# Kernel optimization log

Measured on AMD Instinct MI355X. Metric: run time of the kernel, lower is better.

## Reference

```python
import jax, jax.numpy as jnp
import numpy as np
from jax import lax

B, H, W, C, NH = 16, 56, 56, 192, 6
L = H * W
DH = C // NH            # 32
HID = 4 * C             # 768
ETA = 1.0 / DH          # TTT inner-loop learning rate
EPS = 1e-5

# ---- RoPE rotation tables (deterministic buffer, shape (H, W, C//2)) ----
_kmax = C // 4
_theta = 1.0 / (10000.0 ** (np.arange(_kmax) / _kmax))
_ii, _jj = np.meshgrid(np.arange(H), np.arange(W), indexing='ij')
_ang = np.concatenate([_ii[..., None] * _theta, _jj[..., None] * _theta], axis=-1)  # (H,W,C/2)
_COS = jnp.asarray(np.cos(_ang), dtype=jnp.float32)
_SIN = jnp.asarray(np.sin(_ang), dtype=jnp.float32)


def layernorm(x, g, b):
    mu = jnp.mean(x, axis=-1, keepdims=True)
    var = jnp.mean(jnp.square(x - mu), axis=-1, keepdims=True)
    return (x - mu) * lax.rsqrt(var + EPS) * g + b


def dwconv3x3(x_blc, w, b):
    # x: (B, L, Ch) -> depthwise 3x3 conv over (H, W) -> (B, L, Ch)
    Ch = x_blc.shape[-1]
    xi = x_blc.reshape(B, H, W, Ch).transpose(0, 3, 1, 2)  # NCHW
    y = lax.conv_general_dilated(xi, w, (1, 1), 'SAME', feature_group_count=Ch,
                                 dimension_numbers=('NCHW', 'OIHW', 'NCHW'))
    y = y + b[None, :, None, None]
    return y.transpose(0, 2, 3, 1).reshape(B, L, Ch)


def rope(x):
    # x: (B, L, C); rotate complex pairs with 2D axial angles
    xr = x.reshape(B, H, W, C // 2, 2)
    re, im = xr[..., 0], xr[..., 1]
    o_re = _COS * re - _SIN * im
    o_im = _SIN * re + _COS * im
    return jnp.stack([o_re, o_im], axis=-1).reshape(B, L, C)


def ttt_attn(xn, qkv_w, qkv_b, W0, proj_w, proj_b):
    qkv = xn @ qkv_w.T + qkv_b                      # (B, L, 3C)
    q, k, v = jnp.split(qkv, 3, axis=-1)
    q = rope(q) * (DH ** -0.5)
    k = rope(k)

    def to_heads(t):  # (B,L,C) -> (L, B*NH, DH)
        return t.reshape(B, L, NH, DH).transpose(1, 0, 2, 3).reshape(L, B * NH, DH)
    qs, ks, vs = to_heads(q), to_heads(k), to_heads(v)

    Wst0 = jnp.broadcast_to(W0[None], (B, NH, DH, DH)).reshape(B * NH, DH, DH)

    def step(Wst, qkv_t):
        qt, kt, vt = qkv_t
        pred = jnp.einsum('bij,bj->bi', Wst, kt)
        Wn = Wst - ETA * (pred - vt)[:, :, None] * kt[:, None, :]
        ot = jnp.einsum('bij,bj->bi', Wn, qt)
        return Wn, ot

    _, out = lax.scan(step, Wst0, (qs, ks, vs))     # out: (L, B*NH, DH)
    out = out.reshape(L, B, NH, DH).transpose(1, 0, 2, 3).reshape(B, L, C)
    return out @ proj_w.T + proj_b


def setup_inputs() -> dict:
    key = jax.random.key(0)
    ks = jax.random.split(key, 12)
    s = 0.02
    return {
        'x': jax.random.normal(ks[0], (B, L, C), jnp.float32),
        'cpe_w': jax.random.normal(ks[1], (C, 1, 3, 3), jnp.float32) * s,
        'cpe_b': jnp.zeros((C,), jnp.float32),
        'n1_g': jnp.ones((C,), jnp.float32),
        'n1_b': jnp.zeros((C,), jnp.float32),
        'qkv_w': jax.random.normal(ks[2], (3 * C, C), jnp.float32) * s,
        'qkv_b': jnp.zeros((3 * C,), jnp.float32),
        'W0': jax.random.normal(ks[3], (NH, DH, DH), jnp.float32) * s,
        'proj_w': jax.random.normal(ks[4], (C, C), jnp.float32) * s,
        'proj_b': jnp.zeros((C,), jnp.float32),
        'n2_g': jnp.ones((C,), jnp.float32),
        'n2_b': jnp.zeros((C,), jnp.float32),
        'fc1_w': jax.random.normal(ks[5], (HID, C), jnp.float32) * s,
        'fc1_b': jnp.zeros((HID,), jnp.float32),
        'dwc_w': jax.random.normal(ks[6], (HID, 1, 3, 3), jnp.float32) * s,
        'dwc_b': jnp.zeros((HID,), jnp.float32),
        'fc2_w': jax.random.normal(ks[7], (C, HID), jnp.float32) * s,
        'fc2_b': jnp.zeros((C,), jnp.float32),
    }


def reference(x, cpe_w, cpe_b, n1_g, n1_b, qkv_w, qkv_b, W0, proj_w, proj_b,
              n2_g, n2_b, fc1_w, fc1_b, dwc_w, dwc_b, fc2_w, fc2_b):
    # CPE: conditional positional encoding (depthwise conv residual)
    x = x + dwconv3x3(x, cpe_w, cpe_b)
    # TTT attention branch
    x = x + ttt_attn(layernorm(x, n1_g, n1_b), qkv_w, qkv_b, W0, proj_w, proj_b)
    # MLP branch with depthwise conv
    h1 = jax.nn.gelu(layernorm(x, n2_g, n2_b) @ fc1_w.T + fc1_b, approximate=False)
    h1 = jax.nn.gelu(h1 + dwconv3x3(h1, dwc_w, dwc_b), approximate=False)
    x = x + (h1 @ fc2_w.T + fc2_b)
    return x
```

## Files before the change

kernel.cpp:

```cpp
#include <hip/hip_runtime.h>
#include <hip/hip_bf16.h>

#define Bc 16
#define Hc 56
#define Wcc 56
#define Cc 192
#define NHc 6
#define Lc 3136
#define DHc 32
#define HIDc 768
#define NHEAD 96
#define Sc 32
#define NCHUNK 98
#define NPAIR (NHEAD*NCHUNK)
#define ROWS (Bc*Lc)
#define GR2 (ROWS/2)
#define ETAc (1.0f/32.0f)

typedef unsigned short u16;
typedef unsigned int u32;
typedef __attribute__((ext_vector_type(8))) short bf16x8;
typedef __attribute__((ext_vector_type(4))) float f32x4;
typedef __attribute__((ext_vector_type(16))) float f32x16;

__device__ __forceinline__ float b2f(u16 v){ u32 u = ((u32)v)<<16; float f; __builtin_memcpy(&f,&u,4); return f; }
__device__ __forceinline__ u16 f2b(float f){ u32 u; __builtin_memcpy(&u,&f,4); u32 r = u + 0x7FFFu + ((u>>16)&1u); return (u16)(r>>16); }
__device__ __forceinline__ f32x16 zero16(){ f32x16 z = {0,0,0,0,0,0,0,0,0,0,0,0,0,0,0,0}; return z; }

__device__ __forceinline__ void make_bfrags(const f32x16& t, int hi, bf16x8& b1, bf16x8& b2){
  u32 P[8], S[8];
  #pragma unroll
  for (int q=0;q<4;q++){
    #pragma unroll
    for (int j=0;j<2;j++){
      u32 r; float lo = t[4*q+2*j], hv = t[4*q+2*j+1];
      asm("v_cvt_pk_bf16_f32 %0, %1, %2" : "=v"(r) : "v"(lo), "v"(hv));
      P[2*q+j] = r;
    }
  }
  #pragma unroll
  for (int i=0;i<8;i++) S[i] = (u32)__shfl_xor((int)P[i], 32);
  union { u32 u[4]; bf16x8 v; } f1, f2;
  if (hi==0){ f1.u[0]=P[0]; f1.u[1]=P[1]; f1.u[2]=S[0]; f1.u[3]=S[1];
              f2.u[0]=P[4]; f2.u[1]=P[5]; f2.u[2]=S[4]; f2.u[3]=S[5]; }
  else      { f1.u[0]=S[2]; f1.u[1]=S[3]; f1.u[2]=P[2]; f1.u[3]=P[3];
              f2.u[0]=S[6]; f2.u[1]=S[7]; f2.u[2]=P[6]; f2.u[3]=P[7]; }
  b1 = f1.v; b2 = f2.v;
}

__global__ __launch_bounds__(256) void prep_kernel(
    const float* __restrict__ qkvw, const float* __restrict__ projw,
    const float* __restrict__ fc1w, const float* __restrict__ fc2w,
    const float* __restrict__ dwcw, const float* __restrict__ cpew,
    u16* __restrict__ wbqkv, u16* __restrict__ wbproj, u16* __restrict__ wbfc1,
    u16* __restrict__ wbfc2, float* __restrict__ dwt9, float* __restrict__ cwt9){
  int i = blockIdx.x*256 + threadIdx.x;
  if (i < 110592) wbqkv[i] = f2b(qkvw[i]);
  else if (i < 147456){ int j=i-110592; wbproj[j] = f2b(projw[j]); }
  else if (i < 294912){ int j=i-147456; wbfc1[j] = f2b(fc1w[j]); }
  else if (i < 442368){ int j=i-294912; wbfc2[j] = f2b(fc2w[j]); }
  else if (i < 449280){ int j=i-442368; int ch=j/9, t=j-ch*9; dwt9[t*HIDc+ch] = dwcw[j]; }
  else if (i < 451008){ int j=i-449280; int ch=j/9, t=j-ch*9; cwt9[t*Cc+ch] = cpew[j]; }
}

__global__ __launch_bounds__(256) void rope_tab_kernel(float* __restrict__ ct, float* __restrict__ st){
  int i = blockIdx.x*256 + threadIdx.x;
  int l = i/96, p = i - l*96;
  int h = l/Wcc, w = l - h*Wcc;
  int kk = (p<48)? p : p-48;
  float th = powf(10000.f, -(float)kk/48.f);
  float ang = (float)((p<48)? h : w) * th;
  ct[i] = cosf(ang);
  st[i] = sinf(ang);
}

__global__ __launch_bounds__(192) void cpe_ln_kernel(const float* __restrict__ x, const float* __restrict__ cwt9,
                                                     const float* __restrict__ bs, const float* __restrict__ g,
                                                     const float* __restrict__ b,
                                                     u16* __restrict__ x1, u16* __restrict__ xn){
  __shared__ float ps[192], pq[192], smu[8], srs[8];
  int tid = threadIdx.x;
  int rl = tid/24, sub = tid - rl*24, ch0 = sub*8;
  int row = blockIdx.x*8 + rl;
  int l = row % Lc; int h = l/Wcc, w = l - h*Wcc;
  const float* xp = x + (size_t)row*Cc + ch0;
  float acc[8];
  { f32x4 b0 = *(const f32x4*)(bs+ch0), b1v = *(const f32x4*)(bs+ch0+4);
    acc[0]=b0[0];acc[1]=b0[1];acc[2]=b0[2];acc[3]=b0[3];
    acc[4]=b1v[0];acc[5]=b1v[1];acc[6]=b1v[2];acc[7]=b1v[3]; }
  #pragma unroll
  for (int kh=0;kh<3;kh++){
    int hh = h+kh-1; if (hh<0 || hh>=Hc) continue;
    #pragma unroll
    for (int kw=0;kw<3;kw++){
      int ww = w+kw-1; if (ww<0 || ww>=Wcc) continue;
      const float* ip = xp + ((kh-1)*Wcc + (kw-1))*Cc;
      f32x4 i0 = *(const f32x4*)ip, i1 = *(const f32x4*)(ip+4);
      const float* wp = cwt9 + (kh*3+kw)*Cc + ch0;
      f32x4 w0 = *(const f32x4*)wp, w1 = *(const f32x4*)(wp+4);
      acc[0] += i0[0]*w0[0]; acc[1] += i0[1]*w0[1]; acc[2] += i0[2]*w0[2]; acc[3] += i0[3]*w0[3];
      acc[4] += i1[0]*w1[0]; acc[5] += i1[1]*w1[1]; acc[6] += i1[2]*w1[2]; acc[7] += i1[3]*w1[3];
    }
  }
  float val[8];
  { f32x4 c0 = *(const f32x4*)xp, c1 = *(const f32x4*)(xp+4);
    val[0]=c0[0]+acc[0]; val[1]=c0[1]+acc[1]; val[2]=c0[2]+acc[2]; val[3]=c0[3]+acc[3];
    val[4]=c1[0]+acc[4]; val[5]=c1[1]+acc[5]; val[6]=c1[2]+acc[6]; val[7]=c1[3]+acc[7]; }
  float s8=0.f, q8=0.f;
  #pragma unroll
  for (int j=0;j<8;j++){ s8 += val[j]; q8 += val[j]*val[j]; }
  ps[tid]=s8; pq[tid]=q8;
  __syncthreads();
  if (tid < 8){
    float s=0.f, q=0.f;
    #pragma unroll
    for (int k=0;k<24;k++){ s += ps[tid*24+k]; q += pq[tid*24+k]; }
    float mu = s*(1.f/Cc);
    float var = q*(1.f/Cc) - mu*mu;
    smu[tid] = mu; srs[tid] = rsqrtf(var + 1e-5f);
  }
  __syncthreads();
  float mu = smu[rl], rstd = srs[rl];
  union { bf16x8 v; u16 s[8]; } o1, o2;
  f32x4 g0 = *(const f32x4*)(g+ch0), g1 = *(const f32x4*)(g+ch0+4);
  f32x4 bb0 = *(const f32x4*)(b+ch0), bb1 = *(const f32x4*)(b+ch0+4);
  float gg[8] = {g0[0],g0[1],g0[2],g0[3],g1[0],g1[1],g1[2],g1[3]};
  float bbv[8] = {bb0[0],bb0[1],bb0[2],bb0[3],bb1[0],bb1[1],bb1[2],bb1[3]};
  #pragma unroll
  for (int j=0;j<8;j++){
    o1.s[j] = f2b(val[j]);
    o2.s[j] = f2b((val[j]-mu)*rstd*gg[j] + bbv[j]);
  }
  *(bf16x8*)(x1 + (size_t)row*Cc + ch0) = o1.v;
  *(bf16x8*)(xn + (size_t)row*Cc + ch0) = o2.v;
}

__global__ __launch_bounds__(256) void ln_kernel(const u16* __restrict__ xb, const float* __restrict__ g,
                                                 const float* __restrict__ b, u16* __restrict__ out){
  int row = blockIdx.x*4 + (threadIdx.x>>6);
  int lane = threadIdx.x & 63;
  const u16* xr = xb + (size_t)row*Cc;
  float v0 = b2f(xr[lane]), v1 = b2f(xr[lane+64]), v2 = b2f(xr[lane+128]);
  float s = v0+v1+v2;
  float q = v0*v0 + v1*v1 + v2*v2;
  #pragma unroll
  for (int off=32; off; off>>=1){ s += __shfl_xor(s, off); q += __shfl_xor(q, off); }
  float mu = s*(1.f/Cc);
  float var = q*(1.f/Cc) - mu*mu;
  float rstd = rsqrtf(var + 1e-5f);
  u16* orow = out + (size_t)row*Cc;
  orow[lane]     = f2b((v0-mu)*rstd*g[lane]     + b[lane]);
  orow[lane+64]  = f2b((v1-mu)*rstd*g[lane+64]  + b[lane+64]);
  orow[lane+128] = f2b((v2-mu)*rstd*g[lane+128] + b[lane+128]);
}

template<int MODE, int KT>
__global__ __launch_bounds__(256) void gemm_kernel(
    const u16* __restrict__ A, const u16* __restrict__ Wt,
    const float* __restrict__ bias,
    float* __restrict__ outf, u16* __restrict__ outb, u16* __restrict__ vdst,
    const u16* __restrict__ residb,
    const float* __restrict__ ct, const float* __restrict__ st,
    u16* __restrict__ q_s, u16* __restrict__ k_s)
{
  constexpr int NCH = KT/192;
  __shared__ __align__(16) char smem[64*200*2];
  u16* As = (u16*)smem;
  float* Os32 = (float*)smem;
  u16* Osu = (u16*)smem;
  int tid = threadIdx.x;
  int wid = tid>>6, lane = tid&63;
  int wr = wid>>1, wc = wid&1;
  int m0 = blockIdx.x*64;
  int nblk = blockIdx.y*192;
  int n0 = nblk + wc*96;
  int ar = lane&15, kg = lane>>4;
  f32x4 acc[2][6];
  #pragma unroll
  for (int f=0;f<2;f++)
    #pragma unroll
    for (int c=0;c<6;c++){ f32x4 z = {0.f,0.f,0.f,0.f}; acc[f][c] = z; }
  bf16x8 bcur[6], bnxt[6];
  #pragma unroll
  for (int c=0;c<6;c++) bcur[c] = *(const bf16x8*)(Wt + (size_t)(n0 + c*16 + ar)*KT + kg*8);
  #pragma unroll
  for (int ch=0; ch<NCH; ch++){
    if (ch>0) __syncthreads();
    #pragma unroll
    for (int j=0;j<6;j++){
      int g = j*256 + tid;
      int grow = g/24, gcol = (g - grow*24)*8;
      bf16x8 v = *(const bf16x8*)(A + (size_t)(m0+grow)*KT + ch*192 + gcol);
      *(bf16x8*)(As + grow*200 + gcol) = v;
    }
    __syncthreads();
    #pragma unroll
    for (int kc=0;kc<6;kc++){
      int s = ch*6 + kc;
      if (s+1 < NCH*6){
        int koff = ((s+1)/6)*192 + ((s+1)%6)*32 + kg*8;
        #pragma unroll
        for (int c=0;c<6;c++) bnxt[c] = *(const bf16x8*)(Wt + (size_t)(n0 + c*16 + ar)*KT + koff);
      }
      bf16x8 af[2];
      #pragma unroll
      for (int f=0;f<2;f++)
        af[f] = *(const bf16x8*)(As + (wr*32 + f*16 + ar)*200 + kc*32 + kg*8);
      #pragma unroll
      for (int f=0;f<2;f++)
        #pragma unroll
        for (int c=0;c<6;c++)
          acc[f][c] = __builtin_amdgcn_mfma_f32_16x16x32_bf16(af[f], bcur[c], acc[f][c], 0,0,0);
      #pragma unroll
      for (int c=0;c<6;c++) bcur[c] = bnxt[c];
    }
  }
  __syncthreads();
  if (MODE != 3){
    #pragma unroll
    for (int f=0;f<2;f++){
      #pragma unroll
      for (int c=0;c<6;c++){
        float bv = bias[n0 + c*16 + ar];
        #pragma unroll
        for (int j=0;j<4;j++){
          float v = acc[f][c][j] + bv;
          if (MODE==2) v = 0.5f*v*(1.f + erff(v*0.70710678118654752f));
          Osu[(wr*32 + f*16 + kg*4 + j)*200 + wc*96 + c*16 + ar] = f2b(v);
        }
      }
    }
    __syncthreads();
    #pragma unroll
    for (int j=0;j<6;j++){
      int g = j*256 + tid;
      int grow = g/24, gcol = (g - grow*24)*8;
      bf16x8 v = *(const bf16x8*)(Osu + grow*200 + gcol);
      int row = m0 + grow;
      if (MODE==2){
        *(bf16x8*)(outb + (size_t)row*HIDc + nblk + gcol) = v;
      } else if (MODE==1){
        const u16* rp = residb + (size_t)row*Cc + gcol;
        bf16x8 rv = *(const bf16x8*)rp;
        union { bf16x8 v; u16 s[8]; } o;
        #pragma unroll
        for (int t=0;t<8;t++) o.s[t] = f2b(b2f((u16)v[t]) + b2f((u16)rv[t]));
        *(bf16x8*)(outb + (size_t)row*Cc + gcol) = o.v;
      } else {
        int bb = row/Lc; int l = row - bb*Lc;
        int nh = gcol>>5, d = gcol&31;
        if (nblk < 384){
          bool isq = (nblk == 0);
          int p0 = gcol>>1;
          f32x4 cv = *(const f32x4*)(ct + l*96 + p0);
          f32x4 sv = *(const f32x4*)(st + l*96 + p0);
          float sc = isq ? 0.1767766952966369f : 1.0f;
          union { bf16x8 v; u16 s[8]; } o;
          #pragma unroll
          for (int t=0;t<4;t++){
            float re = b2f((u16)v[2*t]), im = b2f((u16)v[2*t+1]);
            o.s[2*t]   = f2b((cv[t]*re - sv[t]*im)*sc);
            o.s[2*t+1] = f2b((sv[t]*re + cv[t]*im)*sc);
          }
          u16* dst = (isq ? q_s : k_s) + (((size_t)(bb*NHc+nh))*Lc + l)*DHc + d;
          *(bf16x8*)dst = o.v;
        } else {
          *(bf16x8*)(vdst + (((size_t)(bb*NHc+nh))*Lc + l)*DHc + d) = v;
        }
      }
    }
  } else {
    #pragma unroll
    for (int half=0; half<2; half++){
      if (wc==half){
        #pragma unroll
        for (int f=0;f<2;f++){
          #pragma unroll
          for (int c=0;c<6;c++){
            float bv = bias[n0 + c*16 + ar];
            #pragma unroll
            for (int j=0;j<4;j++)
              Os32[(wr*32 + f*16 + kg*4 + j)*100 + c*16 + ar] = acc[f][c][j] + bv;
          }
        }
      }
      __syncthreads();
      #pragma unroll
      for (int j=0;j<6;j++){
        int g = j*256 + tid;
        int grow = g/24, qcol = (g - grow*24)*4;
        f32x4 v = *(const f32x4*)(Os32 + grow*100 + qcol);
        int row = m0 + grow, colg = half*96 + qcol;
        const u16* rp = residb + (size_t)row*Cc + colg;
        v[0] += b2f(rp[0]); v[1] += b2f(rp[1]); v[2] += b2f(rp[2]); v[3] += b2f(rp[3]);
        *(f32x4*)(outf + (size_t)row*Cc + colg) = v;
      }
      if (half==0) __syncthreads();
    }
  }
}

__global__ __launch_bounds__(64) void ttta_kernel(const u16* __restrict__ k_s, const u16* __restrict__ v_s,
                                                  u16* __restrict__ u_s, u16* __restrict__ rn_s,
                                                  u16* __restrict__ af_s, u16* __restrict__ bc_s){
  __shared__ float Gl[1024];
  __shared__ u16 LK[32*40];
  __shared__ float LU[32*33];
  __shared__ float LR[32*33];
  int pair = blockIdx.x;
  int head = pair / NCHUNK;
  int l0 = (pair - head*NCHUNK) * Sc;
  int lane = threadIdx.x; int rr = lane&31; int hi = lane>>5; int ks = hi*8;
  const u16* kb = k_s + ((size_t)head*Lc + l0)*DHc;
  bf16x8 a0 = *(const bf16x8*)(kb + rr*32 + ks);
  bf16x8 a1 = *(const bf16x8*)(kb + rr*32 + 16 + ks);
  *(bf16x8*)(LK + rr*40 + ks) = a0;
  *(bf16x8*)(LK + rr*40 + 16 + ks) = a1;
  f32x16 g = zero16();
  g = __builtin_amdgcn_mfma_f32_32x32x16_bf16(a0, a0, g, 0,0,0);
  g = __builtin_amdgcn_mfma_f32_32x32x16_bf16(a1, a1, g, 0,0,0);
  #pragma unroll
  for (int reg=0;reg<16;reg++){
    int i = (reg&3) + 8*(reg>>2) + 4*hi;
    Gl[i*32 + rr] = ETAc * g[reg];
  }
  __syncthreads();
  float X[32];
  if (lane < 32){
    #pragma unroll
    for (int i=0;i<32;i++) X[i] = ETAc * b2f(v_s[((size_t)head*Lc + l0 + i)*DHc + lane]);
  } else {
    int m = lane-32;
    #pragma unroll
    for (int i=0;i<32;i++) X[i] = ETAc * b2f(kb[i*32 + m]);
  }
  #pragma unroll
  for (int i=1;i<32;i++){
    float a = X[i];
    #pragma unroll
    for (int j=0;j<i;j++) a -= Gl[i*32+j]*X[j];
    X[i] = a;
  }
  if (lane < 32){
    u16* dst = u_s + (size_t)pair*1024 + lane;
    #pragma unroll
    for (int i=0;i<32;i++) dst[i*32] = f2b(X[i]);
    #pragma unroll
    for (int i=0;i<32;i++) LU[lane*33 + i] = X[i];
  } else {
    u16* dst = rn_s + (size_t)pair*1024 + (lane&31);
    #pragma unroll
    for (int i=0;i<32;i++) dst[i*32] = f2b(-X[i]);
    #pragma unroll
    for (int i=0;i<32;i++) LR[(lane&31)*33 + i] = X[i];
  }
  __syncthreads();
  union { bf16x8 v; u16 s[8]; } kc1, kc2, uc1, uc2, rc1, rc2;
  #pragma unroll
  for (int s=0;s<8;s++){
    kc1.s[s] = LK[(ks+s)*40 + rr];
    kc2.s[s] = LK[(16+ks+s)*40 + rr];
    uc1.s[s] = f2b(LU[rr*33 + ks+s]);
    uc2.s[s] = f2b(LU[rr*33 + 16+ks+s]);
    rc1.s[s] = f2b(LR[rr*33 + ks+s]);
    rc2.s[s] = f2b(LR[rr*33 + 16+ks+s]);
  }
  f32x16 bacc = zero16();
  bacc = __builtin_amdgcn_mfma_f32_32x32x16_bf16(kc1.v, uc1.v, bacc, 0,0,0);
  bacc = __builtin_amdgcn_mfma_f32_32x32x16_bf16(kc2.v, uc2.v, bacc, 0,0,0);
  union { bf16x8 v; u16 s[8]; } bo1, bo2;
  #pragma unroll
  for (int r=0;r<8;r++){ bo1.s[r] = f2b(bacc[r]); bo2.s[r] = f2b(bacc[8+r]); }
  *(bf16x8*)(bc_s + (size_t)pair*1024 + lane*16) = bo1.v;
  *(bf16x8*)(bc_s + (size_t)pair*1024 + lane*16 + 8) = bo2.v;
  f32x16 aacc = zero16();
  aacc = __builtin_amdgcn_mfma_f32_32x32x16_bf16(rc1.v, kc1.v, aacc, 0,0,0);
  aacc = __builtin_amdgcn_mfma_f32_32x32x16_bf16(rc2.v, kc2.v, aacc, 0,0,0);
  f32x16 an;
  #pragma unroll
  for (int r=0;r<16;r++) an[r] = -aacc[r];
  bf16x8 f1, f2;
  make_bfrags(an, hi, f1, f2);
  *(bf16x8*)(af_s + (size_t)pair*1024 + lane*16) = f1;
  *(bf16x8*)(af_s + (size_t)pair*1024 + lane*16 + 8) = f2;
}

__global__ __launch_bounds__(64) void tttb_kernel(const u16* __restrict__ af_s, const u16* __restrict__ bc_s,
                                                  const float* __restrict__ W0, u16* __restrict__ w_snap){
  int head = blockIdx.x; int nh = head % NHc;
  int lane = threadIdx.x; int rr = lane&31; int hi = lane>>5;
  f32x16 T;
  const float* w0r = W0 + nh*1024 + rr*32 + 4*hi;
  #pragma unroll
  for (int q=0;q<4;q++){
    f32x4 v = *(const f32x4*)(w0r + 8*q);
    T[4*q+0]=v[0]; T[4*q+1]=v[1]; T[4*q+2]=v[2]; T[4*q+3]=v[3];
  }
  size_t hb = (size_t)head*NCHUNK;
  const bf16x8* afp = (const bf16x8*)(af_s + hb*1024);
  const bf16x8* bcp = (const bf16x8*)(bc_s + hb*1024);
  bf16x8 A1 = afp[lane*2], A2 = afp[lane*2+1];
  bf16x8 Bv1 = bcp[lane*2], Bv2 = bcp[lane*2+1];
  bf16x8 b1, b2;
  make_bfrags(T, hi, b1, b2);
  for (int c=0;c<NCHUNK;c++){
    bf16x8 nA1=A1, nA2=A2, nB1=Bv1, nB2=Bv2;
    if (c+1 < NCHUNK){
      int base = (c+1)*128 + lane*2;
      nA1 = afp[base]; nA2 = afp[base+1];
      nB1 = bcp[base]; nB2 = bcp[base+1];
    }
    u16* wrow = w_snap + (hb + c)*1024 + rr*32;
    *(bf16x8*)(wrow + hi*8) = b1;
    *(bf16x8*)(wrow + 16 + hi*8) = b2;
    f32x16 acc;
    #pragma unroll
    for (int r=0;r<8;r++){ acc[r] = T[r] + b2f((u16)Bv1[r]); acc[8+r] = T[8+r] + b2f((u16)Bv2[r]); }
    acc = __builtin_amdgcn_mfma_f32_32x32x16_bf16(A1, b1, acc, 0,0,0);
    acc = __builtin_amdgcn_mfma_f32_32x32x16_bf16(A2, b2, acc, 0,0,0);
    T = acc;
    make_bfrags(T, hi, b1, b2);
    A1=nA1; A2=nA2; Bv1=nB1; Bv2=nB2;
  }
}

__global__ __launch_bounds__(64) void tttc_kernel(const u16* __restrict__ q_s, const u16* __restrict__ k_s,
                                                  const u16* __restrict__ w_snap, const u16* __restrict__ u_s,
                                                  const u16* __restrict__ rn_s, u16* __restrict__ o_bf){
  __shared__ __align__(16) u16 Pl[32*40];
  int pair = blockIdx.x;
  int head = pair / NCHUNK;
  int ch = pair - head*NCHUNK;
  int l0 = ch*Sc;
  int lane = threadIdx.x; int rr = lane&31; int hi = lane>>5; int ks = hi*8;
  const u16* qb = q_s + ((size_t)head*Lc + l0)*DHc;
  const u16* kb = k_s + ((size_t)head*Lc + l0)*DHc;
  bf16x8 q0 = *(const bf16x8*)(qb + rr*32 + ks);
  bf16x8 q1 = *(const bf16x8*)(qb + rr*32 + 16 + ks);
  bf16x8 k0 = *(const bf16x8*)(kb + rr*32 + ks);
  bf16x8 k1 = *(const bf16x8*)(kb + rr*32 + 16 + ks);
  f32x16 p = zero16();
  p = __builtin_amdgcn_mfma_f32_32x32x16_bf16(q0, k0, p, 0,0,0);
  p = __builtin_amdgcn_mfma_f32_32x32x16_bf16(q1, k1, p, 0,0,0);
  #pragma unroll
  for (int reg=0;reg<16;reg++){
    int i = (reg&3)+8*(reg>>2)+4*hi;
    Pl[i*40+rr] = (rr<=i) ? f2b(p[reg]) : (u16)0;
  }
  const u16* wsb = w_snap + (size_t)pair*1024;
  bf16x8 tb0 = *(const bf16x8*)(wsb + rr*32 + ks);
  bf16x8 tb1 = *(const bf16x8*)(wsb + rr*32 + 16 + ks);
  const u16* ub = u_s + (size_t)pair*1024;
  f32x16 wr;
  #pragma unroll
  for (int r=0;r<16;r++){
    int i = (r&3)+8*(r>>2)+4*hi;
    wr[r] = b2f(ub[i*32 + rr]);
  }
  const u16* rb = rn_s + (size_t)pair*1024;
  bf16x8 rn0 = *(const bf16x8*)(rb + rr*32 + ks);
  bf16x8 rn1 = *(const bf16x8*)(rb + rr*32 + 16 + ks);
  wr = __builtin_amdgcn_mfma_f32_32x32x16_bf16(rn0, tb0, wr, 0,0,0);
  wr = __builtin_amdgcn_mfma_f32_32x32x16_bf16(rn1, tb1, wr, 0,0,0);
  bf16x8 wb0, wb1;
  make_bfrags(wr, hi, wb0, wb1);
  __syncthreads();
  f32x16 o = zero16();
  o = __builtin_amdgcn_mfma_f32_32x32x16_bf16(q0, tb0, o, 0,0,0);
  o = __builtin_amdgcn_mfma_f32_32x32x16_bf16(q1, tb1, o, 0,0,0);
  bf16x8 pa0 = *(const bf16x8*)(Pl + rr*40 + ks);
  bf16x8 pa1 = *(const bf16x8*)(Pl + rr*40 + 16 + ks);
  o = __builtin_amdgcn_mfma_f32_32x32x16_bf16(pa0, wb0, o, 0,0,0);
  o = __builtin_amdgcn_mfma_f32_32x32x16_bf16(pa1, wb1, o, 0,0,0);
  int bb = head/NHc, nh = head - bb*NHc;
  #pragma unroll
  for (int reg=0;reg<16;reg++){
    int i = (reg&3)+8*(reg>>2)+4*hi;
    o_bf[((size_t)(bb*Lc + l0 + i))*Cc + nh*32 + rr] = f2b(o[reg]);
  }
}

__global__ __launch_bounds__(256) void dwc_kernel(const u16* __restrict__ h1, const float* __restrict__ wt9,
                                                  const float* __restrict__ bs, u16* __restrict__ h2, int row0){
  int gid = blockIdx.x*256 + threadIdx.x;
  int cg = gid % 96; int lrow = gid / 96; int ch0 = cg*8;
  int row = row0 + lrow;
  int l = row % Lc; int h = l/Wcc, w = l - h*Wcc;
  const u16* hp = h1 + (size_t)lrow*HIDc + ch0;
  float acc[8];
  { f32x4 b0 = *(const f32x4*)(bs+ch0), b1v = *(const f32x4*)(bs+ch0+4);
    acc[0]=b0[0];acc[1]=b0[1];acc[2]=b0[2];acc[3]=b0[3];
    acc[4]=b1v[0];acc[5]=b1v[1];acc[6]=b1v[2];acc[7]=b1v[3]; }
  #pragma unroll
  for (int kh=0;kh<3;kh++){
    int hh = h+kh-1; if (hh<0 || hh>=Hc) continue;
    #pragma unroll
    for (int kw=0;kw<3;kw++){
      int ww = w+kw-1; if (ww<0 || ww>=Wcc) continue;
      bf16x8 iv = *(const bf16x8*)(hp + ((kh-1)*Wcc + (kw-1))*HIDc);
      const float* wp = wt9 + (kh*3+kw)*HIDc + ch0;
      f32x4 w0 = *(const f32x4*)wp, w1 = *(const f32x4*)(wp+4);
      acc[0] += b2f((u16)iv[0])*w0[0]; acc[1] += b2f((u16)iv[1])*w0[1];
      acc[2] += b2f((u16)iv[2])*w0[2]; acc[3] += b2f((u16)iv[3])*w0[3];
      acc[4] += b2f((u16)iv[4])*w1[0]; acc[5] += b2f((u16)iv[5])*w1[1];
      acc[6] += b2f((u16)iv[6])*w1[2]; acc[7] += b2f((u16)iv[7])*w1[3];
    }
  }
  bf16x8 cv = *(const bf16x8*)hp;
  union { bf16x8 v; u16 s[8]; } ov;
  #pragma unroll
  for (int j=0;j<8;j++){
    float v = b2f((u16)cv[j]) + acc[j];
    ov.s[j] = f2b(0.5f*v*(1.f + erff(v*0.70710678118654752f)));
  }
  *(bf16x8*)(h2 + (size_t)lrow*HIDc + ch0) = ov.v;
}

extern "C" void kernel_launch(void* const* d_in, const int* in_sizes, int n_in,
                              void* d_out, int out_size, void* d_ws, size_t ws_size,
                              hipStream_t stream){
  const float* x     = (const float*)d_in[0];
  const float* cpe_w = (const float*)d_in[1];
  const float* cpe_b = (const float*)d_in[2];
  const float* n1_g  = (const float*)d_in[3];
  const float* n1_b  = (const float*)d_in[4];
  const float* qkv_w = (const float*)d_in[5];
  const float* qkv_b = (const float*)d_in[6];
  const float* W0    = (const float*)d_in[7];
  const float* proj_w= (const float*)d_in[8];
  const float* proj_b= (const float*)d_in[9];
  const float* n2_g  = (const float*)d_in[10];
  const float* n2_b  = (const float*)d_in[11];
  const float* fc1_w = (const float*)d_in[12];
  const float* fc1_b = (const float*)d_in[13];
  const float* dwc_w = (const float*)d_in[14];
  const float* dwc_b = (const float*)d_in[15];
  const float* fc2_w = (const float*)d_in[16];
  const float* fc2_b = (const float*)d_in[17];

  char* ws = (char*)d_ws;
  size_t off = 0;
  auto alloc = [&](size_t bytes)->char*{
    char* p = ws + off;
    off += (bytes + 255) & ~(size_t)255;
    return p;
  };
  u16* wbqkv = (u16*)alloc((size_t)576*192*2);
  u16* wbproj= (u16*)alloc((size_t)192*192*2);
  u16* wbfc1 = (u16*)alloc((size_t)768*192*2);
  u16* wbfc2 = (u16*)alloc((size_t)192*768*2);
  float* dwt9 = (float*)alloc((size_t)9*HIDc*4);
  float* cwt9 = (float*)alloc((size_t)9*Cc*4);
  float* ctab = (float*)alloc((size_t)Lc*96*4);
  float* stab = (float*)alloc((size_t)Lc*96*4);
  u16* regA = (u16*)alloc((size_t)ROWS*Cc*2);
  u16* regB = (u16*)alloc((size_t)ROWS*Cc*2);
  u16* regC = (u16*)alloc((size_t)NHEAD*Lc*DHc*2);
  u16* regD = (u16*)alloc((size_t)NHEAD*Lc*DHc*2);
  u16* regE = (u16*)alloc((size_t)NHEAD*Lc*DHc*2);
  u16* rn_s = (u16*)alloc((size_t)NPAIR*1024*2);
  u16* af_s = (u16*)alloc((size_t)NPAIR*1024*2);
  u16* us = (u16*)d_out;
  u16* bc = us + (size_t)NPAIR*1024;

  u16* x1 = regA;
  u16* x2b = regA;
  u16* xn = regB;
  u16* obf = regB;
  u16* xn2 = regB;
  u16* qs = regC;
  u16* vs = regD;
  u16* wsn = regD;
  u16* ksb = regE;
  u16* h1 = regD;
  u16* h2 = rn_s;

  prep_kernel<<<(451008+255)/256,256,0,stream>>>(qkv_w, proj_w, fc1_w, fc2_w, dwc_w, cpe_w,
                                                 wbqkv, wbproj, wbfc1, wbfc2, dwt9, cwt9);
  rope_tab_kernel<<<(Lc*96)/256,256,0,stream>>>(ctab, stab);

  cpe_ln_kernel<<<ROWS/8,192,0,stream>>>(x, cwt9, cpe_b, n1_g, n1_b, x1, xn);
  { dim3 g(ROWS/64, 3); gemm_kernel<0,192><<<g,256,0,stream>>>(xn, wbqkv, qkv_b,
      nullptr, nullptr, vs, nullptr, ctab, stab, qs, ksb); }
  ttta_kernel<<<NPAIR,64,0,stream>>>(ksb, vs, us, rn_s, af_s, bc);
  tttb_kernel<<<NHEAD,64,0,stream>>>(af_s, bc, W0, wsn);
  tttc_kernel<<<NPAIR,64,0,stream>>>(qs, ksb, wsn, us, rn_s, obf);
  { dim3 g(ROWS/64, 1); gemm_kernel<1,192><<<g,256,0,stream>>>(obf, wbproj, proj_b,
      nullptr, x2b, nullptr, x1, nullptr, nullptr, nullptr, nullptr); }
  ln_kernel<<<ROWS/4,256,0,stream>>>(x2b, n2_g, n2_b, xn2);
  for (int g4=0; g4<2; g4++){
    const u16* a_in = xn2 + (size_t)g4*GR2*Cc;
    float* xo = (float*)d_out + (size_t)g4*GR2*Cc;
    const u16* res = x2b + (size_t)g4*GR2*Cc;
    { dim3 g(GR2/64, 4); gemm_kernel<2,192><<<g,256,0,stream>>>(a_in, wbfc1, fc1_b,
        nullptr, h1, nullptr, nullptr, nullptr, nullptr, nullptr, nullptr); }
    dwc_kernel<<<(GR2*96)/256,256,0,stream>>>(h1, dwt9, dwc_b, h2, g4*GR2);
    { dim3 g(GR2/64, 1); gemm_kernel<3,768><<<g,256,0,stream>>>(h2, wbfc2, fc2_b,
        xo, nullptr, nullptr, res, nullptr, nullptr, nullptr, nullptr); }
  }
}
```

Baseline: 503.3 us.

## Fuse depthwise conv into fc2 GEMM and loop N-blocks inside GEMM blocks

The standalone depthwise-conv+GELU kernel is folded into the fc2 GEMM: each 32-row block computes the conv output for all 768 channels directly into shared memory and then runs the K=768 MFMA loop from there. This removes the h2 round trip through global memory and one launch per half. The generic GEMM now loads its A tile once and loops over all N-blocks (3 for qkv, 4 for fc1) inside one block, so A is not reloaded per grid column. The cost is fewer, longer blocks, a larger shared-memory footprint that may lower occupancy, and 32-row fc2 tiles with less MFMA reuse.

```diff
diff --git a/kernel.cpp b/kernel.cpp
--- a/kernel.cpp
+++ b/kernel.cpp
@@ -154,53 +154,46 @@
   orow[lane+128] = f2b((v2-mu)*rstd*g[lane+128] + b[lane+128]);
 }
 
-template<int MODE, int KT>
+template<int MODE, int NB>
 __global__ __launch_bounds__(256) void gemm_kernel(
     const u16* __restrict__ A, const u16* __restrict__ Wt,
     const float* __restrict__ bias,
-    float* __restrict__ outf, u16* __restrict__ outb, u16* __restrict__ vdst,
+    u16* __restrict__ outb, u16* __restrict__ vdst,
     const u16* __restrict__ residb,
     const float* __restrict__ ct, const float* __restrict__ st,
     u16* __restrict__ q_s, u16* __restrict__ k_s)
 {
-  constexpr int NCH = KT/192;
-  __shared__ __align__(16) char smem[64*200*2];
-  u16* As = (u16*)smem;
-  float* Os32 = (float*)smem;
-  u16* Osu = (u16*)smem;
+  __shared__ __align__(16) u16 As[64*200];
+  __shared__ __align__(16) u16 Osu[64*200];
   int tid = threadIdx.x;
   int wid = tid>>6, lane = tid&63;
   int wr = wid>>1, wc = wid&1;
   int m0 = blockIdx.x*64;
-  int nblk = blockIdx.y*192;
-  int n0 = nblk + wc*96;
   int ar = lane&15, kg = lane>>4;
-  f32x4 acc[2][6];
-  #pragma unroll
-  for (int f=0;f<2;f++)
-    #pragma unroll
-    for (int c=0;c<6;c++){ f32x4 z = {0.f,0.f,0.f,0.f}; acc[f][c] = z; }
-  bf16x8 bcur[6], bnxt[6];
-  #pragma unroll
-  for (int c=0;c<6;c++) bcur[c] = *(const bf16x8*)(Wt + (size_t)(n0 + c*16 + ar)*KT + kg*8);
-  #pragma unroll
-  for (int ch=0; ch<NCH; ch++){
-    if (ch>0) __syncthreads();
-    #pragma unroll
-    for (int j=0;j<6;j++){
-      int g = j*256 + tid;
-      int grow = g/24, gcol = (g - grow*24)*8;
-      bf16x8 v = *(const bf16x8*)(A + (size_t)(m0+grow)*KT + ch*192 + gcol);
-      *(bf16x8*)(As + grow*200 + gcol) = v;
-    }
-    __syncthreads();
+  #pragma unroll
+  for (int j=0;j<6;j++){
+    int g = j*256 + tid;
+    int grow = g/24, gcol = (g - grow*24)*8;
+    *(bf16x8*)(As + grow*200 + gcol) = *(const bf16x8*)(A + (size_t)(m0+grow)*192 + gcol);
+  }
+  __syncthreads();
+  #pragma unroll
+  for (int nb=0; nb<NB; nb++){
+    const int nblk = nb*192;
+    const int n0 = nblk + wc*96;
+    f32x4 acc[2][6];
+    #pragma unroll
+    for (int f=0;f<2;f++)
+      #pragma unroll
+      for (int c=0;c<6;c++){ f32x4 z={0.f,0.f,0.f,0.f}; acc[f][c]=z; }
+    bf16x8 bcur[6], bnxt[6];
+    #pragma unroll
+    for (int c=0;c<6;c++) bcur[c] = *(const bf16x8*)(Wt + (size_t)(n0 + c*16 + ar)*192 + kg*8);
     #pragma unroll
     for (int kc=0;kc<6;kc++){
-      int s = ch*6 + kc;
-      if (s+1 < NCH*6){
-        int koff = ((s+1)/6)*192 + ((s+1)%6)*32 + kg*8;
+      if (kc < 5){
         #pragma unroll
-        for (int c=0;c<6;c++) bnxt[c] = *(const bf16x8*)(Wt + (size_t)(n0 + c*16 + ar)*KT + koff);
+        for (int c=0;c<6;c++) bnxt[c] = *(const bf16x8*)(Wt + (size_t)(n0 + c*16 + ar)*192 + (kc+1)*32 + kg*8);
       }
       bf16x8 af[2];
       #pragma unroll
@@ -214,9 +207,7 @@
       #pragma unroll
       for (int c=0;c<6;c++) bcur[c] = bnxt[c];
     }
-  }
-  __syncthreads();
-  if (MODE != 3){
+    __syncthreads();
     #pragma unroll
     for (int f=0;f<2;f++){
       #pragma unroll
@@ -240,8 +231,7 @@
       if (MODE==2){
         *(bf16x8*)(outb + (size_t)row*HIDc + nblk + gcol) = v;
       } else if (MODE==1){
-        const u16* rp = residb + (size_t)row*Cc + gcol;
-        bf16x8 rv = *(const bf16x8*)rp;
+        bf16x8 rv = *(const bf16x8*)(residb + (size_t)row*Cc + gcol);
         union { bf16x8 v; u16 s[8]; } o;
         #pragma unroll
         for (int t=0;t<8;t++) o.s[t] = f2b(b2f((u16)v[t]) + b2f((u16)rv[t]));
@@ -249,8 +239,8 @@
       } else {
         int bb = row/Lc; int l = row - bb*Lc;
         int nh = gcol>>5, d = gcol&31;
-        if (nblk < 384){
-          bool isq = (nblk == 0);
+        if (nb < 2){
+          const bool isq = (nb == 0);
           int p0 = gcol>>1;
           f32x4 cv = *(const f32x4*)(ct + l*96 + p0);
           f32x4 sv = *(const f32x4*)(st + l*96 + p0);
@@ -269,33 +259,99 @@
         }
       }
     }
-  } else {
-    #pragma unroll
-    for (int half=0; half<2; half++){
-      if (wc==half){
+  }
+}
+
+__global__ __launch_bounds__(256) void dwcfc2_kernel(
+    const u16* __restrict__ h1, const float* __restrict__ wt9, const float* __restrict__ dbs,
+    const u16* __restrict__ Wt, const float* __restrict__ bias,
+    const u16* __restrict__ residb, float* __restrict__ outf)
+{
+  __shared__ __align__(16) u16 As[32*776];
+  __shared__ __align__(16) float Os32[32*100];
+  int tid = threadIdx.x;
+  int wid = tid>>6, lane = tid&63;
+  int wr = wid>>1, wc = wid&1;
+  int m0 = blockIdx.x*32;
+  int n0 = wc*96;
+  int ar = lane&15, kg = lane>>4;
+  #pragma unroll
+  for (int j=0;j<12;j++){
+    int g = j*256 + tid;
+    int grow = g/96, gcol = (g - grow*96)*8;
+    int row = m0 + grow;
+    int l = row % Lc; int h = l/Wcc, w = l - h*Wcc;
+    const u16* hp = h1 + (size_t)row*HIDc + gcol;
+    float acc[8];
+    { f32x4 b0 = *(const f32x4*)(dbs+gcol), b1v = *(const f32x4*)(dbs+gcol+4);
+      acc[0]=b0[0];acc[1]=b0[1];acc[2]=b0[2];acc[3]=b0[3];
+      acc[4]=b1v[0];acc[5]=b1v[1];acc[6]=b1v[2];acc[7]=b1v[3]; }
+    #pragma unroll
+    for (int kh=0;kh<3;kh++){
+      int hh = h+kh-1; if (hh<0 || hh>=Hc) continue;
+      #pragma unroll
+      for (int kw=0;kw<3;kw++){
+        int ww = w+kw-1; if (ww<0 || ww>=Wcc) continue;
+        bf16x8 iv = *(const bf16x8*)(hp + ((kh-1)*Wcc + (kw-1))*HIDc);
+        const float* wp = wt9 + (kh*3+kw)*HIDc + gcol;
+        f32x4 w0 = *(const f32x4*)wp, w1 = *(const f32x4*)(wp+4);
+        acc[0] += b2f((u16)iv[0])*w0[0]; acc[1] += b2f((u16)iv[1])*w0[1];
+        acc[2] += b2f((u16)iv[2])*w0[2]; acc[3] += b2f((u16)iv[3])*w0[3];
+        acc[4] += b2f((u16)iv[4])*w1[0]; acc[5] += b2f((u16)iv[5])*w1[1];
+        acc[6] += b2f((u16)iv[6])*w1[2]; acc[7] += b2f((u16)iv[7])*w1[3];
+      }
+    }
+    bf16x8 cv = *(const bf16x8*)hp;
+    union { bf16x8 v; u16 s[8]; } ov;
+    #pragma unroll
+    for (int t=0;t<8;t++){
+      float v = b2f((u16)cv[t]) + acc[t];
+      ov.s[t] = f2b(0.5f*v*(1.f + erff(v*0.70710678118654752f)));
+    }
+    *(bf16x8*)(As + grow*776 + gcol) = ov.v;
+  }
+  __syncthreads();
+  f32x4 acc[6];
+  #pragma unroll
+  for (int c=0;c<6;c++){ f32x4 z={0.f,0.f,0.f,0.f}; acc[c]=z; }
+  bf16x8 bcur[6], bnxt[6];
+  #pragma unroll
+  for (int c=0;c<6;c++) bcur[c] = *(const bf16x8*)(Wt + (size_t)(n0 + c*16 + ar)*HIDc + kg*8);
+  #pragma unroll
+  for (int ks=0; ks<24; ks++){
+    if (ks < 23){
+      #pragma unroll
+      for (int c=0;c<6;c++) bnxt[c] = *(const bf16x8*)(Wt + (size_t)(n0 + c*16 + ar)*HIDc + (ks+1)*32 + kg*8);
+    }
+    bf16x8 af = *(const bf16x8*)(As + (wr*16 + ar)*776 + ks*32 + kg*8);
+    #pragma unroll
+    for (int c=0;c<6;c++)
+      acc[c] = __builtin_amdgcn_mfma_f32_16x16x32_bf16(af, bcur[c], acc[c], 0,0,0);
+    #pragma unroll
+    for (int c=0;c<6;c++) bcur[c] = bnxt[c];
+  }
+  #pragma unroll
+  for (int half=0; half<2; half++){
+    __syncthreads();
+    if (wc==half){
+      #pragma unroll
+      for (int c=0;c<6;c++){
+        float bv = bias[n0 + c*16 + ar];
         #pragma unroll
-        for (int f=0;f<2;f++){
-          #pragma unroll
-          for (int c=0;c<6;c++){
-            float bv = bias[n0 + c*16 + ar];
-            #pragma unroll
-            for (int j=0;j<4;j++)
-              Os32[(wr*32 + f*16 + kg*4 + j)*100 + c*16 + ar] = acc[f][c][j] + bv;
-          }
-        }
+        for (int j=0;j<4;j++)
+          Os32[(wr*16 + kg*4 + j)*100 + c*16 + ar] = acc[c][j] + bv;
       }
-      __syncthreads();
-      #pragma unroll
-      for (int j=0;j<6;j++){
-        int g = j*256 + tid;
-        int grow = g/24, qcol = (g - grow*24)*4;
-        f32x4 v = *(const f32x4*)(Os32 + grow*100 + qcol);
-        int row = m0 + grow, colg = half*96 + qcol;
-        const u16* rp = residb + (size_t)row*Cc + colg;
-        v[0] += b2f(rp[0]); v[1] += b2f(rp[1]); v[2] += b2f(rp[2]); v[3] += b2f(rp[3]);
-        *(f32x4*)(outf + (size_t)row*Cc + colg) = v;
-      }
-      if (half==0) __syncthreads();
+    }
+    __syncthreads();
+    #pragma unroll
+    for (int j=0;j<3;j++){
+      int g = j*256 + tid;
+      int grow = g/24, qcol = (g - grow*24)*4;
+      f32x4 v = *(const f32x4*)(Os32 + grow*100 + qcol);
+      int row = m0 + grow, colg = half*96 + qcol;
+      const u16* rp = residb + (size_t)row*Cc + colg;
+      v[0] += b2f(rp[0]); v[1] += b2f(rp[1]); v[2] += b2f(rp[2]); v[3] += b2f(rp[3]);
+      *(f32x4*)(outf + (size_t)row*Cc + colg) = v;
     }
   }
 }
@@ -478,42 +534,6 @@
     int i = (reg&3)+8*(reg>>2)+4*hi;
     o_bf[((size_t)(bb*Lc + l0 + i))*Cc + nh*32 + rr] = f2b(o[reg]);
   }
-}
-
-__global__ __launch_bounds__(256) void dwc_kernel(const u16* __restrict__ h1, const float* __restrict__ wt9,
-                                                  const float* __restrict__ bs, u16* __restrict__ h2, int row0){
-  int gid = blockIdx.x*256 + threadIdx.x;
-  int cg = gid % 96; int lrow = gid / 96; int ch0 = cg*8;
-  int row = row0 + lrow;
-  int l = row % Lc; int h = l/Wcc, w = l - h*Wcc;
-  const u16* hp = h1 + (size_t)lrow*HIDc + ch0;
-  float acc[8];
-  { f32x4 b0 = *(const f32x4*)(bs+ch0), b1v = *(const f32x4*)(bs+ch0+4);
-    acc[0]=b0[0];acc[1]=b0[1];acc[2]=b0[2];acc[3]=b0[3];
-    acc[4]=b1v[0];acc[5]=b1v[1];acc[6]=b1v[2];acc[7]=b1v[3]; }
-  #pragma unroll
-  for (int kh=0;kh<3;kh++){
-    int hh = h+kh-1; if (hh<0 || hh>=Hc) continue;
-    #pragma unroll
-    for (int kw=0;kw<3;kw++){
-      int ww = w+kw-1; if (ww<0 || ww>=Wcc) continue;
-      bf16x8 iv = *(const bf16x8*)(hp + ((kh-1)*Wcc + (kw-1))*HIDc);
-      const float* wp = wt9 + (kh*3+kw)*HIDc + ch0;
-      f32x4 w0 = *(const f32x4*)wp, w1 = *(const f32x4*)(wp+4);
-      acc[0] += b2f((u16)iv[0])*w0[0]; acc[1] += b2f((u16)iv[1])*w0[1];
-      acc[2] += b2f((u16)iv[2])*w0[2]; acc[3] += b2f((u16)iv[3])*w0[3];
-      acc[4] += b2f((u16)iv[4])*w1[0]; acc[5] += b2f((u16)iv[5])*w1[1];
-      acc[6] += b2f((u16)iv[6])*w1[2]; acc[7] += b2f((u16)iv[7])*w1[3];
-    }
-  }
-  bf16x8 cv = *(const bf16x8*)hp;
-  union { bf16x8 v; u16 s[8]; } ov;
-  #pragma unroll
-  for (int j=0;j<8;j++){
-    float v = b2f((u16)cv[j]) + acc[j];
-    ov.s[j] = f2b(0.5f*v*(1.f + erff(v*0.70710678118654752f)));
-  }
-  *(bf16x8*)(h2 + (size_t)lrow*HIDc + ch0) = ov.v;
 }
 
 extern "C" void kernel_launch(void* const* d_in, const int* in_sizes, int n_in,
@@ -573,29 +593,26 @@
   u16* wsn = regD;
   u16* ksb = regE;
   u16* h1 = regD;
-  u16* h2 = rn_s;
 
   prep_kernel<<<(451008+255)/256,256,0,stream>>>(qkv_w, proj_w, fc1_w, fc2_w, dwc_w, cpe_w,
                                                  wbqkv, wbproj, wbfc1, wbfc2, dwt9, cwt9);
   rope_tab_kernel<<<(Lc*96)/256,256,0,stream>>>(ctab, stab);
 
   cpe_ln_kernel<<<ROWS/8,192,0,stream>>>(x, cwt9, cpe_b, n1_g, n1_b, x1, xn);
-  { dim3 g(ROWS/64, 3); gemm_kernel<0,192><<<g,256,0,stream>>>(xn, wbqkv, qkv_b,
-      nullptr, nullptr, vs, nullptr, ctab, stab, qs, ksb); }
+  gemm_kernel<0,3><<<ROWS/64,256,0,stream>>>(xn, wbqkv, qkv_b,
+      nullptr, vs, nullptr, ctab, stab, qs, ksb);
   ttta_kernel<<<NPAIR,64,0,stream>>>(ksb, vs, us, rn_s, af_s, bc);
   tttb_kernel<<<NHEAD,64,0,stream>>>(af_s, bc, W0, wsn);
   tttc_kernel<<<NPAIR,64,0,stream>>>(qs, ksb, wsn, us, rn_s, obf);
-  { dim3 g(ROWS/64, 1); gemm_kernel<1,192><<<g,256,0,stream>>>(obf, wbproj, proj_b,
-      nullptr, x2b, nullptr, x1, nullptr, nullptr, nullptr, nullptr); }
+  gemm_kernel<1,1><<<ROWS/64,256,0,stream>>>(obf, wbproj, proj_b,
+      x2b, nullptr, x1, nullptr, nullptr, nullptr, nullptr);
   ln_kernel<<<ROWS/4,256,0,stream>>>(x2b, n2_g, n2_b, xn2);
   for (int g4=0; g4<2; g4++){
     const u16* a_in = xn2 + (size_t)g4*GR2*Cc;
     float* xo = (float*)d_out + (size_t)g4*GR2*Cc;
     const u16* res = x2b + (size_t)g4*GR2*Cc;
-    { dim3 g(GR2/64, 4); gemm_kernel<2,192><<<g,256,0,stream>>>(a_in, wbfc1, fc1_b,
-        nullptr, h1, nullptr, nullptr, nullptr, nullptr, nullptr, nullptr); }
-    dwc_kernel<<<(GR2*96)/256,256,0,stream>>>(h1, dwt9, dwc_b, h2, g4*GR2);
-    { dim3 g(GR2/64, 1); gemm_kernel<3,768><<<g,256,0,stream>>>(h2, wbfc2, fc2_b,
-        xo, nullptr, nullptr, res, nullptr, nullptr, nullptr, nullptr); }
-  }
-}
+    gemm_kernel<2,4><<<GR2/64,256,0,stream>>>(a_in, wbfc1, fc1_b,
+        h1, nullptr, nullptr, nullptr, nullptr, nullptr, nullptr);
+    dwcfc2_kernel<<<GR2/32,256,0,stream>>>(h1, dwt9, dwc_b, wbfc2, fc2_b, res, xo);
+  }
+}
```

New measurement: 678.6 us. 1.35x slower.
